# Performance work log

Measured on AMD Instinct MI355X. Metric: run time of the kernel, lower is better.

The kernel has to match this reference:

```python
import jax, jax.numpy as jnp
import numpy as np
import math

B, S, H, NS = 64, 1024, 1024, 8
TEMPERATURE = 1.0


def setup_inputs() -> dict:
    key = jax.random.key(0)
    ks = jax.random.split(key, 14)
    sc = 1.0 / math.sqrt(H)
    inp = {
        "x": jax.random.normal(ks[0], (B, S, H), dtype=jnp.float32),
        "Wq": jax.random.normal(ks[1], (H, H), dtype=jnp.float32) * sc,
        "bq": jax.random.normal(ks[2], (H,), dtype=jnp.float32) * sc,
        "Wk": jax.random.normal(ks[3], (H, H), dtype=jnp.float32) * sc,
        "bk": jax.random.normal(ks[4], (H,), dtype=jnp.float32) * sc,
        "Wv": jax.random.normal(ks[5], (H, H), dtype=jnp.float32) * sc,
        "bv": jax.random.normal(ks[6], (H,), dtype=jnp.float32) * sc,
        "Wp": jax.random.normal(ks[7], (NS, H, H), dtype=jnp.float32) * sc,
        "bp": jax.random.normal(ks[8], (NS, H), dtype=jnp.float32) * sc,
        "Ws": jax.random.normal(ks[9], (H, NS), dtype=jnp.float32) * sc,
        "bs": jax.random.normal(ks[10], (NS,), dtype=jnp.float32) * sc,
        "Wo": jax.random.normal(ks[11], (H, H), dtype=jnp.float32) * sc,
        "bo": jax.random.normal(ks[12], (H,), dtype=jnp.float32) * sc,
    }
    return inp


def reference(x, Wq, bq, Wk, bk, Wv, bv, Wp, bp, Ws, bs, Wo, bo):
    b, s_len, h = x.shape
    ns = Wp.shape[0]
    inv_base = 1.0 / math.sqrt(h * TEMPERATURE)
    inv_h = 1.0 / math.sqrt(h)

    x_last = x[:, -1, :]                      # [B,H]
    q = x_last @ Wq + bq                      # [B,H]
    k = x @ Wk + bk                           # [B,S,H]
    v = x @ Wv + bv                           # [B,S,H]

    attn_base = jax.nn.softmax(jnp.einsum("bh,bsh->bs", q, k) * inv_base, axis=-1)
    base_context = jnp.einsum("bs,bsh->bh", attn_base, v)   # [B,H]

    scale_importance = jax.nn.softmax(x_last @ Ws + bs, axis=-1)  # [B,NS]

    combined = jnp.zeros((b, h), dtype=x.dtype)
    for i in range(ns):
        size = max(1, s_len // (2 ** i))
        if size == 1:
            pooled = jnp.mean(x, axis=1, keepdims=True)      # [B,1,H]
        else:
            stride = max(1, size // 2)
            # S divisible by stride; window j = halves j and j+1
            half_sums = x.reshape(b, s_len // stride, stride, h).sum(axis=2)
            pooled = (half_sums[:, :-1] + half_sums[:, 1:]) / size  # [B,nw,H]
        feat = jnp.tanh(pooled @ Wp[i] + bp[i])              # [B,nw,H]
        fa = jax.nn.softmax(jnp.einsum("bh,bnh->bn", q, feat) * inv_h, axis=-1)
        ctx = jnp.einsum("bn,bnh->bh", fa, feat)
        combined = combined + scale_importance[:, i:i + 1] * ctx

    return (base_context + combined) @ Wo + bo
```

## Files before the change

kernel.cpp:

```cpp
#include <hip/hip_runtime.h>
#include <cstdint>
#include <cstddef>

#define BB 64
#define SS 1024
#define HH 1024
#define NSS 8

__device__ __constant__ int PBrow_c[8]    = {0,128,384,896,1920,3968,8064,16256};
__device__ __constant__ int realbase_c[8] = {0,64,256,704,1664,3648,7680,15808};

#define INV32 0.03125f

typedef __attribute__((ext_vector_type(8))) short short8;
typedef __attribute__((ext_vector_type(4))) float f32x4;

__device__ __forceinline__ uint16_t f2bf(float f) {
  union { float f; uint32_t u; } v; v.f = f;
  uint32_t r = v.u + 0x7fffu + ((v.u >> 16) & 1u);
  return (uint16_t)(r >> 16);
}
__device__ __forceinline__ float bf_lo(uint32_t w) { return __uint_as_float(w << 16); }
__device__ __forceinline__ float bf_hi(uint32_t w) { return __uint_as_float(w & 0xffff0000u); }

__device__ __forceinline__ float fast_tanh(float x) {
  const float ax = __builtin_fabsf(x);
  const float t  = __builtin_amdgcn_exp2f(ax * -2.885390081777927f);
  const float r  = (1.0f - t) * __builtin_amdgcn_rcpf(1.0f + t);
  return __builtin_copysignf(r, x);
}

__device__ __forceinline__ void gld_lds16(const void* g, void* l) {
  __builtin_amdgcn_global_load_lds((const __attribute__((address_space(1))) uint32_t*)g,
                                   (__attribute__((address_space(3))) uint32_t*)l, 16, 0, 0);
}

__device__ __forceinline__ size_t pk_idx(int row, int k) {
  return (((size_t)(row >> 7) * 16 + (k >> 6)) * 8 + ((k >> 3) & 7)) * 1024
         + (size_t)(row & 127) * 8 + (k & 7);
}

template<bool TRANSB>
__global__ __launch_bounds__(256) void gemm64(
    const float* __restrict__ A, size_t a_stride,
    const float* __restrict__ W,
    const float* __restrict__ bias,
    const float* __restrict__ addb,
    float* __restrict__ out)
{
  __shared__ float As[64][68];
  __shared__ float Bs[64][68];
  const int t  = threadIdx.x;
  const int nt = blockIdx.x;
  const int ks = blockIdx.y;
  const int m0 = (t >> 4) << 2;
  const int n0 = (t & 15) << 2;
  float acc[4][4] = {};
  for (int kt = 0; kt < 2; ++kt) {
    const int k0 = ks * 128 + kt * 64;
    {
      const int m  = t >> 2;
      const int kb = (t & 3) << 4;
      #pragma unroll
      for (int j = 0; j < 4; ++j) {
        const int k = kb + j * 4;
        const float4 v = *(const float4*)(A + (size_t)m * a_stride + k0 + k);
        As[k+0][m] = v.x; As[k+1][m] = v.y; As[k+2][m] = v.z; As[k+3][m] = v.w;
      }
    }
    if (!TRANSB) {
      const int k  = t >> 2;
      const int nb = (t & 3) << 4;
      #pragma unroll
      for (int j = 0; j < 4; ++j) {
        const int n = nb + j * 4;
        *(float4*)&Bs[k][n] = *(const float4*)(W + (size_t)(k0 + k) * HH + nt * 64 + n);
      }
    } else {
      const int n  = t >> 2;
      const int kb = (t & 3) << 4;
      #pragma unroll
      for (int j = 0; j < 4; ++j) {
        const int k = kb + j * 4;
        const float4 v = *(const float4*)(W + (size_t)(nt * 64 + n) * HH + k0 + k);
        Bs[k+0][n] = v.x; Bs[k+1][n] = v.y; Bs[k+2][n] = v.z; Bs[k+3][n] = v.w;
      }
    }
    __syncthreads();
    #pragma unroll 16
    for (int k = 0; k < 64; ++k) {
      const float4 av = *(const float4*)&As[k][m0];
      const float4 bv = *(const float4*)&Bs[k][n0];
      const float a[4] = {av.x, av.y, av.z, av.w};
      const float b[4] = {bv.x, bv.y, bv.z, bv.w};
      #pragma unroll
      for (int i2 = 0; i2 < 4; ++i2)
        #pragma unroll
        for (int j2 = 0; j2 < 4; ++j2)
          acc[i2][j2] += a[i2] * b[j2];
    }
    __syncthreads();
  }
  #pragma unroll
  for (int i2 = 0; i2 < 4; ++i2) {
    const int m = m0 + i2;
    #pragma unroll
    for (int j2 = 0; j2 < 4; ++j2) {
      const int n = nt * 64 + n0 + j2;
      float v = acc[i2][j2];
      if (ks == 0) {
        if (bias) v += bias[n];
        if (addb) v += addb[(size_t)m * HH + n];
      }
      atomicAdd(out + (size_t)m * HH + n, v);
    }
  }
}

__global__ __launch_bounds__(256) void si_kernel(const float* __restrict__ x,
    const float* __restrict__ Ws, const float* __restrict__ bs,
    float* __restrict__ si)
{
  const int b = blockIdx.x, t = threadIdx.x;
  const int n = t & 7, kc = t >> 3;
  const float* xl = x + ((size_t)b * SS + (SS - 1)) * HH;
  float p = 0.f;
  for (int kk = 0; kk < 32; ++kk) {
    const int k = kc * 32 + kk;
    p += xl[k] * Ws[k * NSS + n];
  }
  __shared__ float red[32][9];
  __shared__ float lg[8];
  red[kc][n] = p;
  __syncthreads();
  if (t < 8) {
    float s2 = bs[t];
    for (int c = 0; c < 32; ++c) s2 += red[c][t];
    lg[t] = s2;
  }
  __syncthreads();
  if (t == 0) {
    float mx = lg[0];
    #pragma unroll
    for (int j = 1; j < 8; ++j) mx = fmaxf(mx, lg[j]);
    float e[8]; float sm = 0.f;
    #pragma unroll
    for (int j = 0; j < 8; ++j) { e[j] = expf(lg[j] - mx); sm += e[j]; }
    const float inv = 1.0f / sm;
    #pragma unroll
    for (int j = 0; j < 8; ++j) si[b * NSS + j] = e[j] * inv;
  }
}

__global__ __launch_bounds__(256) void score_kernel(const float* __restrict__ x,
    const float* __restrict__ qk, float* __restrict__ attn)
{
  const int b = blockIdx.y, sc = blockIdx.x;
  const int t = threadIdx.x;
  const int lane = t & 63, w = t >> 6;
  __shared__ float qks[HH];
  __shared__ float red[8][4];
  *(float4*)&qks[t * 4] = *(const float4*)&qk[b * HH + t * 4];
  __syncthreads();
  for (int ss = 0; ss < 8; ++ss) {
    const int s = sc * 8 + ss;
    const float4 xv = *(const float4*)&x[((size_t)b * SS + s) * HH + t * 4];
    const float4 qv = *(const float4*)&qks[t * 4];
    float p = xv.x * qv.x + xv.y * qv.y + xv.z * qv.z + xv.w * qv.w;
    #pragma unroll
    for (int off = 32; off > 0; off >>= 1) p += __shfl_down(p, off);
    if (lane == 0) red[ss][w] = p;
  }
  __syncthreads();
  if (t < 8) {
    const float v = (red[t][0] + red[t][1] + red[t][2] + red[t][3]) * INV32;
    attn[(size_t)b * SS + sc * 8 + t] = v;
  }
}

__global__ __launch_bounds__(256) void softmax_s(float* __restrict__ attn)
{
  const int b = blockIdx.x, t = threadIdx.x;
  float* row = attn + (size_t)b * SS;
  float4 v = *(float4*)&row[t * 4];
  float mx = fmaxf(fmaxf(v.x, v.y), fmaxf(v.z, v.w));
  #pragma unroll
  for (int off = 32; off > 0; off >>= 1) mx = fmaxf(mx, __shfl_xor(mx, off));
  __shared__ float rm[4];
  __shared__ float rs[4];
  if ((t & 63) == 0) rm[t >> 6] = mx;
  __syncthreads();
  mx = fmaxf(fmaxf(rm[0], rm[1]), fmaxf(rm[2], rm[3]));
  const float e0 = expf(v.x - mx), e1 = expf(v.y - mx), e2 = expf(v.z - mx), e3 = expf(v.w - mx);
  float sm = e0 + e1 + e2 + e3;
  #pragma unroll
  for (int off = 32; off > 0; off >>= 1) sm += __shfl_xor(sm, off);
  if ((t & 63) == 0) rs[t >> 6] = sm;
  __syncthreads();
  sm = rs[0] + rs[1] + rs[2] + rs[3];
  const float inv = 1.0f / sm;
  v.x = e0 * inv; v.y = e1 * inv; v.z = e2 * inv; v.w = e3 * inv;
  *(float4*)&row[t * 4] = v;
}

__global__ __launch_bounds__(256) void pool_kernel(const float* __restrict__ x,
    const float* __restrict__ attn, uint16_t* __restrict__ P,
    float* __restrict__ xa)
{
  const int b = blockIdx.y;
  const int h = blockIdx.x * 256 + threadIdx.x;
  __shared__ float at[SS];
  #pragma unroll
  for (int j = 0; j < 4; ++j) at[threadIdx.x + j * 256] = attn[(size_t)b * SS + threadIdx.x + j * 256];
  __syncthreads();
  const float* xp = x + (size_t)b * SS * HH + h;
  float lacc[8] = {0,0,0,0,0,0,0,0};
  float lprev[8] = {0,0,0,0,0,0,0,0};
  float xacc = 0.f, chunk = 0.f;
  for (int s16 = 0; s16 < 64; ++s16) {
    float v[16];
    #pragma unroll
    for (int j = 0; j < 16; ++j) v[j] = xp[(size_t)(s16 * 16 + j) * HH];
    #pragma unroll
    for (int j = 0; j < 16; ++j) {
      const int s = s16 * 16 + j;
      xacc += at[s] * v[j];
      chunk += v[j];
      if ((j & 3) == 3) {
        const int cidx = s >> 2;
        const float c = chunk; chunk = 0.f;
        #pragma unroll
        for (int L = 0; L < 8; ++L) {
          lacc[L] += c;
          if (((cidx + 1) & ((1 << L) - 1)) == 0) {
            const int mh = ((cidx + 1) >> L) - 1;
            if (mh >= 1) {
              const int i  = 7 - L;
              const int ni = (256 >> L) - 1;
              const int row = PBrow_c[i] + b * ni + (mh - 1);
              const float inv_size = 1.0f / (float)(8 << L);
              P[pk_idx(row, h)] = f2bf((lprev[L] + lacc[L]) * inv_size);
            }
            lprev[L] = lacc[L]; lacc[L] = 0.f;
          }
        }
      }
    }
  }
  xa[(size_t)b * HH + h] = xacc;
}

__global__ __launch_bounds__(256) void wcvt(const float* __restrict__ Wp,
                                            uint16_t* __restrict__ Wpk)
{
  __shared__ float tile[32][33];
  const int s = blockIdx.z;
  const int n0 = blockIdx.x * 32, k0 = blockIdx.y * 32;
  const float* src = Wp + (size_t)s * HH * HH;
  uint16_t* dst = Wpk + (size_t)s * HH * HH;
  const int t = threadIdx.x;
  #pragma unroll
  for (int i = 0; i < 4; ++i) {
    const int kl = i * 8 + (t >> 5), nl = t & 31;
    tile[kl][nl] = src[(size_t)(k0 + kl) * HH + n0 + nl];
  }
  __syncthreads();
  #pragma unroll
  for (int i = 0; i < 4; ++i) {
    const int nl = i * 8 + (t >> 5), kl = t & 31;
    dst[pk_idx(n0 + nl, k0 + kl)] = f2bf(tile[kl][nl]);
  }
}

__global__ __launch_bounds__(256) void feat_gemm(const uint16_t* __restrict__ P,
    const uint16_t* __restrict__ Wpk, const float* __restrict__ bp,
    uint16_t* __restrict__ feat)
{
  __shared__ __align__(16) uint16_t As[8 * 128 * 8];
  __shared__ __align__(16) uint16_t Bs[8 * 128 * 8];
  const int t = threadIdx.x;
  const int w = t >> 6, lane = t & 63;
  const int quad = lane >> 4, l16 = lane & 15;
  const int wg  = blockIdx.y * 8 + blockIdx.x;
  const int lin = (wg & 7) * 255 + (wg >> 3);
  const int ty  = lin >> 3;
  const int ct  = lin & 7;
  const int scale = 31 - __clz(ty + 1);
  const int tloc  = ty - ((1 << scale) - 1);
  const int row0  = PBrow_c[scale] + tloc * 128;
  const int rt    = row0 >> 7;
  const float* bps = bp + scale * HH;
  const int ncol0 = ct * 128;
  const int wm = (w & 1) * 64, wn = (w >> 1) * 64;

  f32x4 acc[4][4];
  #pragma unroll
  for (int mt = 0; mt < 4; ++mt)
    #pragma unroll
    for (int nt = 0; nt < 4; ++nt)
      acc[mt][nt] = (f32x4){0.f, 0.f, 0.f, 0.f};

  const short8* Asv = (const short8*)As;
  const short8* Bsv = (const short8*)Bs;

  for (int kb2 = 0; kb2 < 16; ++kb2) {
    const uint16_t* Ag = P   + ((size_t)(rt * 16 + kb2)) * 8192;
    const uint16_t* Bg = Wpk + ((size_t)((scale * 8 + ct) * 16 + kb2)) * 8192;
    #pragma unroll
    for (int i = w; i < 16; i += 4) {
      gld_lds16(Ag + i * 512 + lane * 8, As + i * 512);
      gld_lds16(Bg + i * 512 + lane * 8, Bs + i * 512);
    }
    __syncthreads();
    #pragma unroll
    for (int ks2 = 0; ks2 < 2; ++ks2) {
      short8 af[4], bf[4];
      #pragma unroll
      for (int mt = 0; mt < 4; ++mt) af[mt] = Asv[(ks2 * 4 + quad) * 128 + wm + mt * 16 + l16];
      #pragma unroll
      for (int nt = 0; nt < 4; ++nt) bf[nt] = Bsv[(ks2 * 4 + quad) * 128 + wn + nt * 16 + l16];
      #pragma unroll
      for (int mt = 0; mt < 4; ++mt)
        #pragma unroll
        for (int nt = 0; nt < 4; ++nt)
          acc[mt][nt] = __builtin_amdgcn_mfma_f32_16x16x32_bf16(af[mt], bf[nt], acc[mt][nt], 0, 0, 0);
    }
    __syncthreads();
  }

  #pragma unroll
  for (int nt = 0; nt < 4; ++nt) {
    const int col = ncol0 + wn + nt * 16 + l16;
    const float bpv = bps[col];
    #pragma unroll
    for (int mt = 0; mt < 4; ++mt) {
      #pragma unroll
      for (int r = 0; r < 4; ++r) {
        const int row = row0 + wm + mt * 16 + quad * 4 + r;
        feat[(size_t)row * HH + col] = f2bf(fast_tanh(acc[mt][nt][r] + bpv));
      }
    }
  }
}

__global__ __launch_bounds__(256) void falogit_kernel(const uint16_t* __restrict__ feat,
    const float* __restrict__ q, float* __restrict__ l)
{
  const int w = threadIdx.x >> 6, lane = threadIdx.x & 63;
  const int r = blockIdx.x * 4 + w;
  int sc = 0;
  #pragma unroll
  for (int i = 1; i < 8; ++i) if (r >= realbase_c[i]) sc = i;
  const int local = r - realbase_c[sc];
  const int ni = (2 << sc) - 1;
  const int b = local / ni;
  const int prow = PBrow_c[sc] + local;
  const uint16_t* fr = feat + (size_t)prow * HH + lane * 16;
  const float*    qr = q + (size_t)b * HH + lane * 16;
  const uint4 f0 = *(const uint4*)fr;
  const uint4 f1 = *(const uint4*)(fr + 8);
  const float4 q0 = *(const float4*)(qr + 0);
  const float4 q1 = *(const float4*)(qr + 4);
  const float4 q2 = *(const float4*)(qr + 8);
  const float4 q3 = *(const float4*)(qr + 12);
  const uint32_t uf[8] = {f0.x, f0.y, f0.z, f0.w, f1.x, f1.y, f1.z, f1.w};
  const float qv[16] = {q0.x,q0.y,q0.z,q0.w, q1.x,q1.y,q1.z,q1.w,
                        q2.x,q2.y,q2.z,q2.w, q3.x,q3.y,q3.z,q3.w};
  float p = 0.f;
  #pragma unroll
  for (int j = 0; j < 8; ++j) {
    p += bf_lo(uf[j]) * qv[2 * j];
    p += bf_hi(uf[j]) * qv[2 * j + 1];
  }
  #pragma unroll
  for (int off = 32; off > 0; off >>= 1) p += __shfl_down(p, off);
  if (lane == 0) l[prow] = p * INV32;
}

__global__ __launch_bounds__(256) void ctx_kernel(const uint16_t* __restrict__ feat,
    const float* __restrict__ l, const float* __restrict__ si,
    float* __restrict__ comb)
{
  const int i = blockIdx.x, b = blockIdx.y, t = threadIdx.x;
  const int ni = (2 << i) - 1;
  const int base = PBrow_c[i] + b * ni;
  __shared__ float fa[256];
  __shared__ float rbuf[4];
  const float lg = (t < ni) ? l[base + t] : -1e30f;
  float mx = lg;
  #pragma unroll
  for (int off = 32; off > 0; off >>= 1) mx = fmaxf(mx, __shfl_xor(mx, off));
  if ((t & 63) == 0) rbuf[t >> 6] = mx;
  __syncthreads();
  mx = fmaxf(fmaxf(rbuf[0], rbuf[1]), fmaxf(rbuf[2], rbuf[3]));
  const float e = (t < ni) ? expf(lg - mx) : 0.f;
  float sm = e;
  #pragma unroll
  for (int off = 32; off > 0; off >>= 1) sm += __shfl_xor(sm, off);
  __syncthreads();
  if ((t & 63) == 0) rbuf[t >> 6] = sm;
  __syncthreads();
  sm = rbuf[0] + rbuf[1] + rbuf[2] + rbuf[3];
  fa[t] = e / sm;
  __syncthreads();
  float c0 = 0.f, c1 = 0.f, c2 = 0.f, c3 = 0.f;
  const int hb = t * 4;
  for (int n = 0; n < ni; ++n) {
    const float fn = fa[n];
    const uint2 u = *(const uint2*)(feat + (size_t)(base + n) * HH + hb);
    c0 += fn * bf_lo(u.x);
    c1 += fn * bf_hi(u.x);
    c2 += fn * bf_lo(u.y);
    c3 += fn * bf_hi(u.y);
  }
  const float sw = si[b * NSS + i];
  atomicAdd(&comb[(size_t)b * HH + hb + 0], sw * c0);
  atomicAdd(&comb[(size_t)b * HH + hb + 1], sw * c1);
  atomicAdd(&comb[(size_t)b * HH + hb + 2], sw * c2);
  atomicAdd(&comb[(size_t)b * HH + hb + 3], sw * c3);
}

extern "C" void kernel_launch(void* const* d_in, const int* in_sizes, int n_in,
                              void* d_out, int out_size, void* d_ws, size_t ws_size,
                              hipStream_t stream) {
  (void)in_sizes; (void)n_in; (void)out_size; (void)ws_size;
  const float* x  = (const float*)d_in[0];
  const float* Wq = (const float*)d_in[1];
  const float* bq = (const float*)d_in[2];
  const float* Wk = (const float*)d_in[3];
  const float* Wv = (const float*)d_in[5];
  const float* bv = (const float*)d_in[6];
  const float* Wp = (const float*)d_in[7];
  const float* bp = (const float*)d_in[8];
  const float* Ws = (const float*)d_in[9];
  const float* bs = (const float*)d_in[10];
  const float* Wo = (const float*)d_in[11];
  const float* bo = (const float*)d_in[12];
  float* out = (float*)d_out;
  char* ws = (char*)d_ws;

  const size_t P_BYTES   = (size_t)32640 * HH * 2;
  const size_t WPT_BYTES = (size_t)NSS * HH * HH * 2;
  uint16_t* P    = (uint16_t*)ws;
  uint16_t* feat = (uint16_t*)(ws + P_BYTES);
  uint16_t* Wpk  = (uint16_t*)(ws + 2 * P_BYTES);
  float* q    = (float*)(ws + 2 * P_BYTES + WPT_BYTES);
  float* qk   = q    + (size_t)BB * HH;
  float* comb = qk   + (size_t)BB * HH;
  float* D    = comb + (size_t)BB * HH;
  float* attn = D    + (size_t)BB * HH;
  float* xa   = attn + (size_t)BB * SS;
  float* si   = xa   + (size_t)BB * HH;
  float* l    = si   + (size_t)BB * NSS;

  hipMemsetAsync(q, 0, (size_t)4 * BB * HH * sizeof(float), stream);
  hipMemsetAsync(d_out, 0, (size_t)BB * HH * sizeof(float), stream);

  wcvt<<<dim3(32, 32, NSS), 256, 0, stream>>>(Wp, Wpk);
  gemm64<false><<<dim3(16, 8), 256, 0, stream>>>(x + (size_t)(SS - 1) * HH, (size_t)SS * HH, Wq, bq, nullptr, q);
  si_kernel<<<BB, 256, 0, stream>>>(x, Ws, bs, si);
  gemm64<true><<<dim3(16, 8), 256, 0, stream>>>(q, (size_t)HH, Wk, nullptr, nullptr, qk);
  score_kernel<<<dim3(128, BB), 256, 0, stream>>>(x, qk, attn);
  softmax_s<<<BB, 256, 0, stream>>>(attn);
  pool_kernel<<<dim3(4, BB), 256, 0, stream>>>(x, attn, P, xa);
  feat_gemm<<<dim3(8, 255), 256, 0, stream>>>(P, Wpk, bp, feat);
  falogit_kernel<<<8032, 256, 0, stream>>>(feat, q, l);
  ctx_kernel<<<dim3(NSS, BB), 256, 0, stream>>>(feat, l, si, comb);
  gemm64<false><<<dim3(16, 8), 256, 0, stream>>>(xa, (size_t)HH, Wv, bv, comb, D);
  gemm64<false><<<dim3(16, 8), 256, 0, stream>>>(D, (size_t)HH, Wo, bo, nullptr, out);
}
```

Measured before the change: 752.4 us.

## Fuse feature-attention logits into feat GEMM epilogue, double-buffer LDS, widen pool unroll

The separate falogit kernel is removed. Its q-dot-feat logit is now computed in the feat_gemm epilogue from the fp32 tanh values, reduced across lanes and accumulated into l with atomicAdd. The batch index comes from a magic-multiply division. The feat GEMM k-loop gets double-buffered LDS so the next tile's global-to-LDS load overlaps the MFMA work. pool_kernel now loads 32 rows per iteration instead of 16. Trade-offs: more registers and LDS (double buffers, the 32-float batch), extra atomics, and a larger memset for l.

New measurement: 790.1 us. 5.0% more time.

```diff
diff --git a/kernel.cpp b/kernel.cpp
--- a/kernel.cpp
+++ b/kernel.cpp
@@ -8,7 +8,8 @@
 #define NSS 8
 
 __device__ __constant__ int PBrow_c[8]    = {0,128,384,896,1920,3968,8064,16256};
-__device__ __constant__ int realbase_c[8] = {0,64,256,704,1664,3648,7680,15808};
+__device__ __constant__ uint32_t minv_c[8] = {0u, 0x55555556u, 0x24924925u, 0x11111112u,
+                                              0x08421085u, 0x04104105u, 0x02040811u, 0x01010102u};
 
 #define INV32 0.03125f
 
@@ -217,13 +218,13 @@
   float lacc[8] = {0,0,0,0,0,0,0,0};
   float lprev[8] = {0,0,0,0,0,0,0,0};
   float xacc = 0.f, chunk = 0.f;
-  for (int s16 = 0; s16 < 64; ++s16) {
-    float v[16];
-    #pragma unroll
-    for (int j = 0; j < 16; ++j) v[j] = xp[(size_t)(s16 * 16 + j) * HH];
-    #pragma unroll
-    for (int j = 0; j < 16; ++j) {
-      const int s = s16 * 16 + j;
+  for (int s32 = 0; s32 < 32; ++s32) {
+    float v[32];
+    #pragma unroll
+    for (int j = 0; j < 32; ++j) v[j] = xp[(size_t)(s32 * 32 + j) * HH];
+    #pragma unroll
+    for (int j = 0; j < 32; ++j) {
+      const int s = s32 * 32 + j;
       xacc += at[s] * v[j];
       chunk += v[j];
       if ((j & 3) == 3) {
@@ -274,10 +275,11 @@
 
 __global__ __launch_bounds__(256) void feat_gemm(const uint16_t* __restrict__ P,
     const uint16_t* __restrict__ Wpk, const float* __restrict__ bp,
-    uint16_t* __restrict__ feat)
-{
-  __shared__ __align__(16) uint16_t As[8 * 128 * 8];
-  __shared__ __align__(16) uint16_t Bs[8 * 128 * 8];
+    const float* __restrict__ q, uint16_t* __restrict__ feat,
+    float* __restrict__ l)
+{
+  __shared__ __align__(16) uint16_t As[2][8 * 128 * 8];
+  __shared__ __align__(16) uint16_t Bs[2][8 * 128 * 8];
   const int t = threadIdx.x;
   const int w = t >> 6, lane = t & 63;
   const int quad = lane >> 4, l16 = lane & 15;
@@ -300,18 +302,23 @@
     for (int nt = 0; nt < 4; ++nt)
       acc[mt][nt] = (f32x4){0.f, 0.f, 0.f, 0.f};
 
-  const short8* Asv = (const short8*)As;
-  const short8* Bsv = (const short8*)Bs;
-
-  for (int kb2 = 0; kb2 < 16; ++kb2) {
+  auto stage = [&](int buf, int kb2) {
     const uint16_t* Ag = P   + ((size_t)(rt * 16 + kb2)) * 8192;
     const uint16_t* Bg = Wpk + ((size_t)((scale * 8 + ct) * 16 + kb2)) * 8192;
     #pragma unroll
     for (int i = w; i < 16; i += 4) {
-      gld_lds16(Ag + i * 512 + lane * 8, As + i * 512);
-      gld_lds16(Bg + i * 512 + lane * 8, Bs + i * 512);
-    }
-    __syncthreads();
+      gld_lds16(Ag + i * 512 + lane * 8, &As[buf][i * 512]);
+      gld_lds16(Bg + i * 512 + lane * 8, &Bs[buf][i * 512]);
+    }
+  };
+
+  stage(0, 0);
+  __syncthreads();
+  int cur = 0;
+  for (int kb2 = 0; kb2 < 16; ++kb2) {
+    if (kb2 < 15) stage(cur ^ 1, kb2 + 1);
+    const short8* Asv = (const short8*)As[cur];
+    const short8* Bsv = (const short8*)Bs[cur];
     #pragma unroll
     for (int ks2 = 0; ks2 < 2; ++ks2) {
       short8 af[4], bf[4];
@@ -326,8 +333,15 @@
           acc[mt][nt] = __builtin_amdgcn_mfma_f32_16x16x32_bf16(af[mt], bf[nt], acc[mt][nt], 0, 0, 0);
     }
     __syncthreads();
-  }
-
+    cur ^= 1;
+  }
+
+  const uint32_t minv = minv_c[scale];
+  float pr[4][4];
+  #pragma unroll
+  for (int mt = 0; mt < 4; ++mt)
+    #pragma unroll
+    for (int r = 0; r < 4; ++r) pr[mt][r] = 0.f;
   #pragma unroll
   for (int nt = 0; nt < 4; ++nt) {
     const int col = ncol0 + wn + nt * 16 + l16;
@@ -337,44 +351,29 @@
       #pragma unroll
       for (int r = 0; r < 4; ++r) {
         const int row = row0 + wm + mt * 16 + quad * 4 + r;
-        feat[(size_t)row * HH + col] = f2bf(fast_tanh(acc[mt][nt][r] + bpv));
-      }
-    }
-  }
-}
-
-__global__ __launch_bounds__(256) void falogit_kernel(const uint16_t* __restrict__ feat,
-    const float* __restrict__ q, float* __restrict__ l)
-{
-  const int w = threadIdx.x >> 6, lane = threadIdx.x & 63;
-  const int r = blockIdx.x * 4 + w;
-  int sc = 0;
-  #pragma unroll
-  for (int i = 1; i < 8; ++i) if (r >= realbase_c[i]) sc = i;
-  const int local = r - realbase_c[sc];
-  const int ni = (2 << sc) - 1;
-  const int b = local / ni;
-  const int prow = PBrow_c[sc] + local;
-  const uint16_t* fr = feat + (size_t)prow * HH + lane * 16;
-  const float*    qr = q + (size_t)b * HH + lane * 16;
-  const uint4 f0 = *(const uint4*)fr;
-  const uint4 f1 = *(const uint4*)(fr + 8);
-  const float4 q0 = *(const float4*)(qr + 0);
-  const float4 q1 = *(const float4*)(qr + 4);
-  const float4 q2 = *(const float4*)(qr + 8);
-  const float4 q3 = *(const float4*)(qr + 12);
-  const uint32_t uf[8] = {f0.x, f0.y, f0.z, f0.w, f1.x, f1.y, f1.z, f1.w};
-  const float qv[16] = {q0.x,q0.y,q0.z,q0.w, q1.x,q1.y,q1.z,q1.w,
-                        q2.x,q2.y,q2.z,q2.w, q3.x,q3.y,q3.z,q3.w};
-  float p = 0.f;
-  #pragma unroll
-  for (int j = 0; j < 8; ++j) {
-    p += bf_lo(uf[j]) * qv[2 * j];
-    p += bf_hi(uf[j]) * qv[2 * j + 1];
-  }
-  #pragma unroll
-  for (int off = 32; off > 0; off >>= 1) p += __shfl_down(p, off);
-  if (lane == 0) l[prow] = p * INV32;
+        const int local = row - PBrow_c[scale];
+        const int b = (scale == 0) ? local
+                    : (int)(((uint64_t)(uint32_t)local * minv) >> 32);
+        const float tv = fast_tanh(acc[mt][nt][r] + bpv);
+        feat[(size_t)row * HH + col] = f2bf(tv);
+        if (b < 64) pr[mt][r] += tv * q[(size_t)b * HH + col];
+      }
+    }
+  }
+  #pragma unroll
+  for (int mt = 0; mt < 4; ++mt) {
+    #pragma unroll
+    for (int r = 0; r < 4; ++r) {
+      float p = pr[mt][r];
+      p += __shfl_xor(p, 1); p += __shfl_xor(p, 2);
+      p += __shfl_xor(p, 4); p += __shfl_xor(p, 8);
+      const int row = row0 + wm + mt * 16 + quad * 4 + r;
+      const int local = row - PBrow_c[scale];
+      const int b = (scale == 0) ? local
+                  : (int)(((uint64_t)(uint32_t)local * minv) >> 32);
+      if (l16 == 0 && b < 64) atomicAdd(&l[row], p * INV32);
+    }
+  }
 }
 
 __global__ __launch_bounds__(256) void ctx_kernel(const uint16_t* __restrict__ feat,
@@ -448,12 +447,12 @@
   float* qk   = q    + (size_t)BB * HH;
   float* comb = qk   + (size_t)BB * HH;
   float* D    = comb + (size_t)BB * HH;
-  float* attn = D    + (size_t)BB * HH;
+  float* l    = D    + (size_t)BB * HH;
+  float* attn = l    + 32640;
   float* xa   = attn + (size_t)BB * SS;
   float* si   = xa   + (size_t)BB * HH;
-  float* l    = si   + (size_t)BB * NSS;
-
-  hipMemsetAsync(q, 0, (size_t)4 * BB * HH * sizeof(float), stream);
+
+  hipMemsetAsync(q, 0, ((size_t)4 * BB * HH + 32640) * sizeof(float), stream);
   hipMemsetAsync(d_out, 0, (size_t)BB * HH * sizeof(float), stream);
 
   wcvt<<<dim3(32, 32, NSS), 256, 0, stream>>>(Wp, Wpk);
@@ -463,8 +462,7 @@
   score_kernel<<<dim3(128, BB), 256, 0, stream>>>(x, qk, attn);
   softmax_s<<<BB, 256, 0, stream>>>(attn);
   pool_kernel<<<dim3(4, BB), 256, 0, stream>>>(x, attn, P, xa);
-  feat_gemm<<<dim3(8, 255), 256, 0, stream>>>(P, Wpk, bp, feat);
-  falogit_kernel<<<8032, 256, 0, stream>>>(feat, q, l);
+  feat_gemm<<<dim3(8, 255), 256, 0, stream>>>(P, Wpk, bp, q, feat, l);
   ctx_kernel<<<dim3(NSS, BB), 256, 0, stream>>>(feat, l, si, comb);
   gemm64<false><<<dim3(16, 8), 256, 0, stream>>>(xa, (size_t)HH, Wv, bv, comb, D);
   gemm64<false><<<dim3(16, 8), 256, 0, stream>>>(D, (size_t)HH, Wo, bo, nullptr, out);
```
